# Performance work log

Hardware: AMD Instinct MI355X
Metric: run time of the kernel (lower is better)

The kernel has to match this reference:

```python
import jax, jax.numpy as jnp
import numpy as np

B, N_BINS, D, G = 2048, 200, 128, 100  # batch, bins (MTL_token_num), feature dim, genes per bin


def setup_inputs() -> dict:
    key = jax.random.key(0)
    k_x, k_w = jax.random.split(key)
    MTL_tokens = jax.random.normal(k_x, (B, N_BINS, D), dtype=jnp.float32)
    # Xavier-uniform init per head: bound = sqrt(6 / (fan_in + fan_out))
    bound = float(np.sqrt(6.0 / (D + G)))
    W = jax.random.uniform(k_w, (N_BINS, G, D), dtype=jnp.float32, minval=-bound, maxval=bound)
    b = jnp.zeros((N_BINS, G), dtype=jnp.float32)
    return {"MTL_tokens": MTL_tokens, "W": W, "b": b}


def reference(MTL_tokens, W, b):
    # Original: for each bin idx, head_idx(MTL_tokens[:, idx]) -> [B, G], collected as a list
    # of length N_BINS, then every scalar is unpacked in (bin, batch, gene) order.
    # Batched grouped GEMM over bins: [B,N,D] x [N,G,D] -> [N,B,G]
    y = jnp.einsum('bnd,ngd->nbg', MTL_tokens, W) + b[:, None, :]
    # activation is None in this config; flatten in (bin, batch, gene) order == the
    # scalar-unpacking double loop of the original module.
    return y.reshape(-1)
```

## Files before the change

### kernel.cpp

```cpp
#include <hip/hip_runtime.h>
#include <hip/hip_bf16.h>

#define NB    200
#define BSZ   2048
#define DD    128
#define GG    100
#define WROWS 112
#define ROWB  256
#define WIMG  (WROWS * ROWB)
#define NTILE (NB * 16)
#define NBLK  512

typedef __attribute__((ext_vector_type(8))) short  short8;
typedef __attribute__((ext_vector_type(4))) float  f32x4;
typedef __attribute__((ext_vector_type(4))) int    i32x4;

__device__ __forceinline__ unsigned f2bf_pack(float lo, float hi) {
    unsigned ulo = __builtin_bit_cast(unsigned, lo);
    ulo += 0x7FFFu + ((ulo >> 16) & 1u);
    unsigned uhi = __builtin_bit_cast(unsigned, hi);
    uhi += 0x7FFFu + ((uhi >> 16) & 1u);
    return (ulo >> 16) | (uhi & 0xFFFF0000u);
}

__device__ __forceinline__ void gload_lds16(const void* g, void* l) {
    __builtin_amdgcn_global_load_lds(
        (const __attribute__((address_space(1))) unsigned int*)g,
        (__attribute__((address_space(3))) unsigned int*)l, 16, 0, 0);
}

#define WAIT_LGKM0() do { asm volatile("" ::: "memory");     \
                          __builtin_amdgcn_s_waitcnt(0xC07F);\
                          __builtin_amdgcn_sched_barrier(0); \
                          __builtin_amdgcn_wave_barrier();   \
                          asm volatile("" ::: "memory"); } while (0)

#define BARRIER_LGKM() do { asm volatile("" ::: "memory");      \
                            __builtin_amdgcn_s_waitcnt(0xC07F); \
                            __builtin_amdgcn_s_barrier();       \
                            __builtin_amdgcn_sched_barrier(0);  \
                            asm volatile("" ::: "memory"); } while (0)

#define BARRIER_VM14() do { asm volatile("s_waitcnt vmcnt(14)" ::: "memory"); \
                            __builtin_amdgcn_s_barrier();        \
                            __builtin_amdgcn_sched_barrier(0);   \
                            asm volatile("" ::: "memory"); } while (0)

#define BARRIER_VM0() do { asm volatile("s_waitcnt vmcnt(0) lgkmcnt(0)" ::: "memory"); \
                           __builtin_amdgcn_s_barrier();        \
                           __builtin_amdgcn_sched_barrier(0);   \
                           asm volatile("" ::: "memory"); } while (0)


__global__ __launch_bounds__(256) void wconv_kernel(
    const float* __restrict__ W, unsigned char* __restrict__ ws)
{
    const int gidx = blockIdx.x * 256 + threadIdx.x;
    if (gidx >= NB * WROWS * 16) return;
    const int gr  = gidx & 15;
    const int row = (gidx >> 4) % WROWS;
    const int n   = gidx / (WROWS * 16);
    i32x4 pack = (i32x4){0, 0, 0, 0};
    if (row < GG) {
        const float* src = W + ((size_t)n * GG + row) * DD + gr * 8;
        const f32x4 a = *reinterpret_cast<const f32x4*>(src);
        const f32x4 b = *reinterpret_cast<const f32x4*>(src + 4);
        pack.x = (int)f2bf_pack(a[0], a[1]);
        pack.y = (int)f2bf_pack(a[2], a[3]);
        pack.z = (int)f2bf_pack(b[0], b[1]);
        pack.w = (int)f2bf_pack(b[2], b[3]);
    }
    const int off = row * ROWB + ((gr * 16) ^ ((row & 7) << 4));
    *reinterpret_cast<i32x4*>(ws + (size_t)n * WIMG + off) = pack;
}

__device__ __forceinline__ void stage_tile(char* buf, const unsigned char* WS,
                                           int n, int lane, int wid) {
    const unsigned char* src = WS + (size_t)n * WIMG;
    #pragma unroll
    for (int i = 0; i < 7; ++i) {
        const int c = i * 4 + wid;
        gload_lds16(src + c * 1024 + lane * 16, buf + c * 1024);
    }
}

__device__ __forceinline__ void load_x(f32x4 (&raw)[2][4][2], const float* X,
                                       int tile, int wid, int l15, int lhi) {
    const int n = tile >> 4;
    const int rowbase = (tile & 15) * 128 + wid * 32;
    #pragma unroll
    for (int rf = 0; rf < 2; ++rf) {
        const float* xrow = X + ((size_t)(rowbase + rf * 16 + l15) * NB + n) * DD + lhi * 8;
        #pragma unroll
        for (int ks = 0; ks < 4; ++ks) {
            raw[rf][ks][0] = *reinterpret_cast<const f32x4*>(xrow + ks * 32);
            raw[rf][ks][1] = *reinterpret_cast<const f32x4*>(xrow + ks * 32 + 4);
        }
    }
}

__device__ __forceinline__ void conv_x(const f32x4 (&raw)[2][4][2],
                                       short8 (&areg)[2][4]) {
    #pragma unroll
    for (int rf = 0; rf < 2; ++rf)
        #pragma unroll
        for (int ks = 0; ks < 4; ++ks) {
            const f32x4 a = raw[rf][ks][0];
            const f32x4 b = raw[rf][ks][1];
            i32x4 pk;
            pk.x = (int)f2bf_pack(a[0], a[1]);
            pk.y = (int)f2bf_pack(a[2], a[3]);
            pk.z = (int)f2bf_pack(b[0], b[1]);
            pk.w = (int)f2bf_pack(b[2], b[3]);
            areg[rf][ks] = __builtin_bit_cast(short8, pk);
        }
}

__device__ __forceinline__ bool tile_body(int tile,
    const float* __restrict__ X, const float* __restrict__ Bias,
    float* __restrict__ Out, const unsigned char* __restrict__ WS,
    char* bufC, char* bufN,
    short8 (&aregC)[2][4], short8 (&aregN)[2][4], f32x4 (&raw)[2][4][2],
    int lane, int wid, int l15, int lhi)
{
    const int n       = tile >> 4;
    const int rowbase = (tile & 15) * 128 + wid * 32;
    const int tn      = tile + NBLK;
    const bool hasnext = (tn < NTILE);

    if (hasnext) {
        stage_tile(bufN, WS, tn >> 4, lane, wid);
        load_x(raw, X, tn, wid, l15, lhi);
    }
    float bias[7];
    #pragma unroll
    for (int cf = 0; cf < 7; ++cf) {
        const int g = cf * 16 + l15;
        bias[cf] = (g < GG) ? Bias[n * GG + g] : 0.0f;
    }

    f32x4 acc[2][7];
    #pragma unroll
    for (int rf = 0; rf < 2; ++rf)
        #pragma unroll
        for (int cf = 0; cf < 7; ++cf)
            acc[rf][cf] = (f32x4){0.f, 0.f, 0.f, 0.f};

    #pragma unroll
    for (int cf = 0; cf < 7; ++cf) {
        const int g    = cf * 16 + l15;
        const int rowb = g * ROWB;
        const int swz  = (g & 7) << 4;
        #pragma unroll
        for (int ks = 0; ks < 4; ++ks) {
            const int off = rowb + (((lhi * 16) + ks * 64) ^ swz);
            const i32x4 braw = *reinterpret_cast<const i32x4*>(bufC + off);
            const short8 bfrag = __builtin_bit_cast(short8, braw);
            acc[0][cf] = __builtin_amdgcn_mfma_f32_16x16x32_bf16(aregC[0][ks], bfrag, acc[0][cf], 0, 0, 0);
            acc[1][cf] = __builtin_amdgcn_mfma_f32_16x16x32_bf16(aregC[1][ks], bfrag, acc[1][cf], 0, 0, 0);
        }
    }

    BARRIER_LGKM();

    float* lds_f = reinterpret_cast<float*>(bufC + wid * 6400);
    #pragma unroll
    for (int rf = 0; rf < 2; ++rf) {
        #pragma unroll
        for (int cf = 0; cf < 7; ++cf) {
            const int g = cf * 16 + l15;
            if (g < GG) {
                #pragma unroll
                for (int j = 0; j < 4; ++j)
                    lds_f[(lhi * 4 + j) * GG + g] = acc[rf][cf][j] + bias[cf];
            }
        }
        WAIT_LGKM0();
        const char* rgn = bufC + wid * 6400;
        char* dst = (char*)(Out + ((size_t)n * BSZ + rowbase + rf * 16) * GG);
        #pragma unroll
        for (int it = 0; it < 7; ++it) {
            const int c = it * 64 + lane;
            if (c < 400) {
                const i32x4 v = *reinterpret_cast<const i32x4*>(rgn + c * 16);
                __builtin_nontemporal_store(v, reinterpret_cast<i32x4*>(dst + c * 16));
            }
        }
        WAIT_LGKM0();
    }

    if (hasnext) conv_x(raw, aregN);

    BARRIER_VM14();
    return hasnext;
}

__global__ __launch_bounds__(256, 2) void mtl_heads_pipe(
    const float* __restrict__ X, const float* __restrict__ Bias,
    const unsigned char* __restrict__ WS, float* __restrict__ Out)
{
    const int tid  = threadIdx.x;
    const int lane = tid & 63;
    const int wid  = tid >> 6;
    const int l15  = lane & 15;
    const int lhi  = lane >> 4;

    __shared__ __align__(16) char smem[2 * WIMG];
    char* bufA = smem;
    char* bufB = smem + WIMG;

    short8 aregA[2][4], aregB[2][4];
    f32x4  raw[2][4][2];

    int t = ((blockIdx.x & 7) << 6) + (blockIdx.x >> 3);

    stage_tile(bufA, WS, t >> 4, lane, wid);
    load_x(raw, X, t, wid, l15, lhi);
    BARRIER_VM0();
    conv_x(raw, aregA);

    for (;;) {
        if (!tile_body(t, X, Bias, Out, WS, bufA, bufB, aregA, aregB, raw,
                       lane, wid, l15, lhi)) break;
        t += NBLK;
        if (!tile_body(t, X, Bias, Out, WS, bufB, bufA, aregB, aregA, raw,
                       lane, wid, l15, lhi)) break;
        t += NBLK;
    }
}

__global__ __launch_bounds__(256, 4) void mtl_heads_fallback(
    const float* __restrict__ X, const float* __restrict__ W,
    const float* __restrict__ Bias, float* __restrict__ Out)
{
    const int n     = blockIdx.y;
    const int mtile = blockIdx.x;
    const int tid   = threadIdx.x;
    const int lane  = tid & 63;
    const int wid   = tid >> 6;
    const int l15   = lane & 15;
    const int lhi   = lane >> 4;

    __shared__ __align__(16) char smem[WIMG];

    {
        const int rsub = tid >> 4;
        const int k0   = (tid & 15) * 8;
        #pragma unroll
        for (int it = 0; it < 7; ++it) {
            const int row = it * 16 + rsub;
            i32x4 pack = (i32x4){0, 0, 0, 0};
            if (row < GG) {
                const float* s = W + ((size_t)n * GG + row) * DD + k0;
                const f32x4 a = *reinterpret_cast<const f32x4*>(s);
                const f32x4 b = *reinterpret_cast<const f32x4*>(s + 4);
                pack.x = (int)f2bf_pack(a[0], a[1]);
                pack.y = (int)f2bf_pack(a[2], a[3]);
                pack.z = (int)f2bf_pack(b[0], b[1]);
                pack.w = (int)f2bf_pack(b[2], b[3]);
            }
            const int off = row * ROWB + ((k0 * 2) ^ ((row & 7) << 4));
            *reinterpret_cast<i32x4*>(smem + off) = pack;
        }
    }

    const int rowbase = mtile * 128 + wid * 32;
    f32x4 raw[2][4][2];
    load_x(raw, X, n * 16 + mtile, wid, l15, lhi);
    float bias[7];
    #pragma unroll
    for (int cf = 0; cf < 7; ++cf) {
        const int g = cf * 16 + l15;
        bias[cf] = (g < GG) ? Bias[n * GG + g] : 0.0f;
    }
    short8 areg[2][4];
    conv_x(raw, areg);

    __syncthreads();

    f32x4 acc[2][7];
    #pragma unroll
    for (int rf = 0; rf < 2; ++rf)
        #pragma unroll
        for (int cf = 0; cf < 7; ++cf)
            acc[rf][cf] = (f32x4){0.f, 0.f, 0.f, 0.f};

    #pragma unroll
    for (int cf = 0; cf < 7; ++cf) {
        const int g    = cf * 16 + l15;
        const int rowb = g * ROWB;
        const int swz  = (g & 7) << 4;
        #pragma unroll
        for (int ks = 0; ks < 4; ++ks) {
            const int off = rowb + (((lhi * 16) + ks * 64) ^ swz);
            const i32x4 braw = *reinterpret_cast<const i32x4*>(smem + off);
            const short8 bfrag = __builtin_bit_cast(short8, braw);
            acc[0][cf] = __builtin_amdgcn_mfma_f32_16x16x32_bf16(areg[0][ks], bfrag, acc[0][cf], 0, 0, 0);
            acc[1][cf] = __builtin_amdgcn_mfma_f32_16x16x32_bf16(areg[1][ks], bfrag, acc[1][cf], 0, 0, 0);
        }
    }

    __syncthreads();

    float* lds_f = reinterpret_cast<float*>(smem + wid * 6400);
    #pragma unroll
    for (int rf = 0; rf < 2; ++rf) {
        #pragma unroll
        for (int cf = 0; cf < 7; ++cf) {
            const int g = cf * 16 + l15;
            if (g < GG) {
                #pragma unroll
                for (int j = 0; j < 4; ++j)
                    lds_f[(lhi * 4 + j) * GG + g] = acc[rf][cf][j] + bias[cf];
            }
        }
        WAIT_LGKM0();
        const char* rgn = smem + wid * 6400;
        char* dst = (char*)(Out + ((size_t)n * BSZ + rowbase + rf * 16) * GG);
        #pragma unroll
        for (int it = 0; it < 7; ++it) {
            const int c = it * 64 + lane;
            if (c < 400) {
                const i32x4 v = *reinterpret_cast<const i32x4*>(rgn + c * 16);
                *reinterpret_cast<i32x4*>(dst + c * 16) = v;
            }
        }
        WAIT_LGKM0();
    }
}

extern "C" void kernel_launch(void* const* d_in, const int* in_sizes, int n_in,
                              void* d_out, int out_size, void* d_ws, size_t ws_size,
                              hipStream_t stream) {
    (void)in_sizes; (void)n_in; (void)out_size;
    const float* X    = (const float*)d_in[0];
    const float* W    = (const float*)d_in[1];
    const float* Bias = (const float*)d_in[2];
    float* Out        = (float*)d_out;
    const size_t wsneed = (size_t)NB * WIMG;
    if (ws_size >= wsneed) {
        wconv_kernel<<<(NB * WROWS * 16 + 255) / 256, 256, 0, stream>>>(W, (unsigned char*)d_ws);
        mtl_heads_pipe<<<dim3(NBLK), 256, 0, stream>>>(X, Bias, (const unsigned char*)d_ws, Out);
    } else {
        mtl_heads_fallback<<<dim3(16, NB), 256, 0, stream>>>(X, W, Bias, Out);
    }
}
```

Before: 73.34 us.

## Assign contiguous tile runs per block to reuse staged bin weights

Each block now handles a contiguous run of 6 or 7 tiles instead of strided tiles spaced NBLK apart. Consecutive tiles mostly share a bin, so the block only stages that bin's weight image into LDS when the bin changes, and reuses it otherwise. The second LDS buffer serves as output scratch, or as the prefetch target when the bin changes. This cuts repeated weight staging traffic per tile, but the prefetch of the next bin's weights is no longer overlapped on every tile, and the per-block workload is slightly uneven.

```diff
diff --git a/kernel.cpp b/kernel.cpp
--- a/kernel.cpp
+++ b/kernel.cpp
@@ -116,86 +116,7 @@
         }
 }
 
-__device__ __forceinline__ bool tile_body(int tile,
-    const float* __restrict__ X, const float* __restrict__ Bias,
-    float* __restrict__ Out, const unsigned char* __restrict__ WS,
-    char* bufC, char* bufN,
-    short8 (&aregC)[2][4], short8 (&aregN)[2][4], f32x4 (&raw)[2][4][2],
-    int lane, int wid, int l15, int lhi)
-{
-    const int n       = tile >> 4;
-    const int rowbase = (tile & 15) * 128 + wid * 32;
-    const int tn      = tile + NBLK;
-    const bool hasnext = (tn < NTILE);
-
-    if (hasnext) {
-        stage_tile(bufN, WS, tn >> 4, lane, wid);
-        load_x(raw, X, tn, wid, l15, lhi);
-    }
-    float bias[7];
-    #pragma unroll
-    for (int cf = 0; cf < 7; ++cf) {
-        const int g = cf * 16 + l15;
-        bias[cf] = (g < GG) ? Bias[n * GG + g] : 0.0f;
-    }
-
-    f32x4 acc[2][7];
-    #pragma unroll
-    for (int rf = 0; rf < 2; ++rf)
-        #pragma unroll
-        for (int cf = 0; cf < 7; ++cf)
-            acc[rf][cf] = (f32x4){0.f, 0.f, 0.f, 0.f};
-
-    #pragma unroll
-    for (int cf = 0; cf < 7; ++cf) {
-        const int g    = cf * 16 + l15;
-        const int rowb = g * ROWB;
-        const int swz  = (g & 7) << 4;
-        #pragma unroll
-        for (int ks = 0; ks < 4; ++ks) {
-            const int off = rowb + (((lhi * 16) + ks * 64) ^ swz);
-            const i32x4 braw = *reinterpret_cast<const i32x4*>(bufC + off);
-            const short8 bfrag = __builtin_bit_cast(short8, braw);
-            acc[0][cf] = __builtin_amdgcn_mfma_f32_16x16x32_bf16(aregC[0][ks], bfrag, acc[0][cf], 0, 0, 0);
-            acc[1][cf] = __builtin_amdgcn_mfma_f32_16x16x32_bf16(aregC[1][ks], bfrag, acc[1][cf], 0, 0, 0);
-        }
-    }
-
-    BARRIER_LGKM();
-
-    float* lds_f = reinterpret_cast<float*>(bufC + wid * 6400);
-    #pragma unroll
-    for (int rf = 0; rf < 2; ++rf) {
-        #pragma unroll
-        for (int cf = 0; cf < 7; ++cf) {
-            const int g = cf * 16 + l15;
-            if (g < GG) {
-                #pragma unroll
-                for (int j = 0; j < 4; ++j)
-                    lds_f[(lhi * 4 + j) * GG + g] = acc[rf][cf][j] + bias[cf];
-            }
-        }
-        WAIT_LGKM0();
-        const char* rgn = bufC + wid * 6400;
-        char* dst = (char*)(Out + ((size_t)n * BSZ + rowbase + rf * 16) * GG);
-        #pragma unroll
-        for (int it = 0; it < 7; ++it) {
-            const int c = it * 64 + lane;
-            if (c < 400) {
-                const i32x4 v = *reinterpret_cast<const i32x4*>(rgn + c * 16);
-                __builtin_nontemporal_store(v, reinterpret_cast<i32x4*>(dst + c * 16));
-            }
-        }
-        WAIT_LGKM0();
-    }
-
-    if (hasnext) conv_x(raw, aregN);
-
-    BARRIER_VM14();
-    return hasnext;
-}
-
-__global__ __launch_bounds__(256, 2) void mtl_heads_pipe(
+__global__ __launch_bounds__(256, 2) void mtl_heads_runs(
     const float* __restrict__ X, const float* __restrict__ Bias,
     const unsigned char* __restrict__ WS, float* __restrict__ Out)
 {
@@ -206,26 +127,90 @@
     const int lhi  = lane >> 4;
 
     __shared__ __align__(16) char smem[2 * WIMG];
-    char* bufA = smem;
-    char* bufB = smem + WIMG;
-
-    short8 aregA[2][4], aregB[2][4];
-    f32x4  raw[2][4][2];
-
-    int t = ((blockIdx.x & 7) << 6) + (blockIdx.x >> 3);
-
-    stage_tile(bufA, WS, t >> 4, lane, wid);
+    char* wbuf = smem;
+    char* obuf = smem + WIMG;
+
+    const int s   = ((blockIdx.x & 7) << 6) + (blockIdx.x >> 3);
+    const int cnt = ((s & 3) == 0) ? 7 : 6;
+    int t = 6 * s + ((s + 3) >> 2);
+
+    stage_tile(wbuf, WS, t >> 4, lane, wid);
+    f32x4 raw[2][4][2];
     load_x(raw, X, t, wid, l15, lhi);
     BARRIER_VM0();
-    conv_x(raw, aregA);
-
-    for (;;) {
-        if (!tile_body(t, X, Bias, Out, WS, bufA, bufB, aregA, aregB, raw,
-                       lane, wid, l15, lhi)) break;
-        t += NBLK;
-        if (!tile_body(t, X, Bias, Out, WS, bufB, bufA, aregB, aregA, raw,
-                       lane, wid, l15, lhi)) break;
-        t += NBLK;
+    short8 areg[2][4];
+    conv_x(raw, areg);
+
+    for (int i = 0; i < cnt; ++i, ++t) {
+        const int  n       = t >> 4;
+        const int  rowbase = (t & 15) * 128 + wid * 32;
+        const bool hasnext = (i + 1 < cnt);
+        const bool binchg  = hasnext && (((t + 1) & 15) == 0);
+
+        if (binchg)  stage_tile(obuf, WS, (t + 1) >> 4, lane, wid);
+        if (hasnext) load_x(raw, X, t + 1, wid, l15, lhi);
+        float bias[7];
+        #pragma unroll
+        for (int cf = 0; cf < 7; ++cf) {
+            const int g = cf * 16 + l15;
+            bias[cf] = (g < GG) ? Bias[n * GG + g] : 0.0f;
+        }
+
+        f32x4 acc[2][7];
+        #pragma unroll
+        for (int rf = 0; rf < 2; ++rf)
+            #pragma unroll
+            for (int cf = 0; cf < 7; ++cf)
+                acc[rf][cf] = (f32x4){0.f, 0.f, 0.f, 0.f};
+
+        #pragma unroll
+        for (int cf = 0; cf < 7; ++cf) {
+            const int g    = cf * 16 + l15;
+            const int rowb = g * ROWB;
+            const int swz  = (g & 7) << 4;
+            #pragma unroll
+            for (int ks = 0; ks < 4; ++ks) {
+                const int off = rowb + (((lhi * 16) + ks * 64) ^ swz);
+                const i32x4 braw = *reinterpret_cast<const i32x4*>(wbuf + off);
+                const short8 bfrag = __builtin_bit_cast(short8, braw);
+                acc[0][cf] = __builtin_amdgcn_mfma_f32_16x16x32_bf16(areg[0][ks], bfrag, acc[0][cf], 0, 0, 0);
+                acc[1][cf] = __builtin_amdgcn_mfma_f32_16x16x32_bf16(areg[1][ks], bfrag, acc[1][cf], 0, 0, 0);
+            }
+        }
+
+        BARRIER_LGKM();
+
+        char* scratch = (binchg ? wbuf : obuf) + wid * 6400;
+        float* lds_f = reinterpret_cast<float*>(scratch);
+        #pragma unroll
+        for (int rf = 0; rf < 2; ++rf) {
+            #pragma unroll
+            for (int cf = 0; cf < 7; ++cf) {
+                const int g = cf * 16 + l15;
+                if (g < GG) {
+                    #pragma unroll
+                    for (int j = 0; j < 4; ++j)
+                        lds_f[(lhi * 4 + j) * GG + g] = acc[rf][cf][j] + bias[cf];
+                }
+            }
+            WAIT_LGKM0();
+            char* dst = (char*)(Out + ((size_t)n * BSZ + rowbase + rf * 16) * GG);
+            #pragma unroll
+            for (int it = 0; it < 7; ++it) {
+                const int c = it * 64 + lane;
+                if (c < 400) {
+                    const i32x4 v = *reinterpret_cast<const i32x4*>(scratch + c * 16);
+                    __builtin_nontemporal_store(v, reinterpret_cast<i32x4*>(dst + c * 16));
+                }
+            }
+            WAIT_LGKM0();
+        }
+
+        if (hasnext) conv_x(raw, areg);
+
+        BARRIER_VM14();
+
+        if (binchg) { char* tmp = wbuf; wbuf = obuf; obuf = tmp; }
     }
 }
 
@@ -340,7 +325,7 @@
     const size_t wsneed = (size_t)NB * WIMG;
     if (ws_size >= wsneed) {
         wconv_kernel<<<(NB * WROWS * 16 + 255) / 256, 256, 0, stream>>>(W, (unsigned char*)d_ws);
-        mtl_heads_pipe<<<dim3(NBLK), 256, 0, stream>>>(X, Bias, (const unsigned char*)d_ws, Out);
+        mtl_heads_runs<<<dim3(NBLK), 256, 0, stream>>>(X, Bias, (const unsigned char*)d_ws, Out);
     } else {
         mtl_heads_fallback<<<dim3(16, NB), 256, 0, stream>>>(X, W, Bias, Out);
     }
```

New measurement: 72.46 us. Within noise of the previous version (-1.2%).
